# Kernel tuning notes

Hardware: AMD Instinct MI355X
Metric: run time of the kernel (lower is better)

## Reference

```python
import jax, jax.numpy as jnp
import numpy as np

B, S, D, H, F = 8, 1024, 1024, 16, 4096
DH = D // H  # 64
EPS = 1e-5


def layer_norm(x, g, b):
    mu = jnp.mean(x, axis=-1, keepdims=True)
    var = jnp.mean(jnp.square(x - mu), axis=-1, keepdims=True)
    return (x - mu) * jax.lax.rsqrt(var + EPS) * g + b


def mha(q_in, k_in, v_in, wq, wk, wv, wo, causal):
    # wq/wk/wv: [H, D, DH] (stacked per-head nn.Linear weights, pre-transposed)
    Q = jnp.einsum('bsd,hdk->bhsk', q_in, wq)
    K = jnp.einsum('bsd,hdk->bhsk', k_in, wk)
    V = jnp.einsum('bsd,hdk->bhsk', v_in, wv)
    scores = jnp.einsum('bhsk,bhtk->bhst', Q, K) / jnp.sqrt(jnp.asarray(DH, Q.dtype))
    if causal:
        mask = jnp.triu(jnp.ones((S, S), dtype=bool), k=1)  # True = inaccessible
        scores = jnp.where(mask, -jnp.inf, scores)
    A = jax.nn.softmax(scores, axis=-1)
    heads = jnp.einsum('bhst,bhtk->bhsk', A, V)
    heads = heads.transpose(0, 2, 1, 3).reshape(q_in.shape[0], q_in.shape[1], D)
    return heads @ wo.T  # nn.Linear convention


def setup_inputs() -> dict:
    key = jax.random.key(0)
    ks = jax.random.split(key, 16)
    sc = 1.0 / np.sqrt(D)
    scf = 1.0 / np.sqrt(F)
    return {
        'embeds': jax.random.normal(ks[0], (B, S, D), jnp.float32),
        'encoder_output': jax.random.normal(ks[1], (B, S, D), jnp.float32),
        'wq1': jax.random.normal(ks[2], (H, D, DH), jnp.float32) * sc,
        'wk1': jax.random.normal(ks[3], (H, D, DH), jnp.float32) * sc,
        'wv1': jax.random.normal(ks[4], (H, D, DH), jnp.float32) * sc,
        'wo1': jax.random.normal(ks[5], (D, D), jnp.float32) * sc,
        'wq2': jax.random.normal(ks[6], (H, D, DH), jnp.float32) * sc,
        'wk2': jax.random.normal(ks[7], (H, D, DH), jnp.float32) * sc,
        'wv2': jax.random.normal(ks[8], (H, D, DH), jnp.float32) * sc,
        'wo2': jax.random.normal(ks[9], (D, D), jnp.float32) * sc,
        'ln1_g': jnp.ones((D,), jnp.float32), 'ln1_b': jnp.zeros((D,), jnp.float32),
        'ln2_g': jnp.ones((D,), jnp.float32), 'ln2_b': jnp.zeros((D,), jnp.float32),
        'ln3_g': jnp.ones((D,), jnp.float32), 'ln3_b': jnp.zeros((D,), jnp.float32),
        'w1': jax.random.normal(ks[10], (F, D), jnp.float32) * sc,
        'b1': jnp.zeros((F,), jnp.float32),
        'w2': jax.random.normal(ks[11], (D, F), jnp.float32) * scf,
        'b2': jnp.zeros((D,), jnp.float32),
    }


def reference(embeds, encoder_output, wq1, wk1, wv1, wo1, wq2, wk2, wv2, wo2,
              ln1_g, ln1_b, ln2_g, ln2_b, ln3_g, ln3_b, w1, b1, w2, b2):
    # masked (causal) self-attention + residual + LN
    sa = mha(embeds, embeds, embeds, wq1, wk1, wv1, wo1, causal=True)
    x1 = layer_norm(sa + embeds, ln1_g, ln1_b)
    # cross-attention (no mask) + residual + LN
    ca = mha(x1, encoder_output, encoder_output, wq2, wk2, wv2, wo2, causal=False)
    x2 = layer_norm(ca + x1, ln2_g, ln2_b)
    # feedforward (Linear -> GELU(exact) -> Linear) + residual + LN
    ff = jax.nn.gelu(x2 @ w1.T + b1, approximate=False) @ w2.T + b2
    return layer_norm(ff + x2, ln3_g, ln3_b)
```

## Files before the change

kernel.cpp:

```cpp
#include <hip/hip_runtime.h>
#include <cstdint>
#include <cstddef>

typedef unsigned short u16;
typedef __attribute__((ext_vector_type(4))) float f32x4;
typedef __attribute__((ext_vector_type(4))) float f4;
typedef __attribute__((ext_vector_type(8))) short short8x;
typedef __attribute__((ext_vector_type(4))) u16 u16x4;
typedef __attribute__((ext_vector_type(8))) u16 u16x8;

#define DEV static __device__ __forceinline__

DEV void gl_lds16(const void* g, void* l) {
  __builtin_amdgcn_global_load_lds(
      (const __attribute__((address_space(1))) unsigned int*)g,
      (__attribute__((address_space(3))) unsigned int*)l, 16, 0, 0);
}

DEV u16 f2bf(float f) {
  unsigned u = __float_as_uint(f);
  u += 0x7fffu + ((u >> 16) & 1u);
  return (u16)(u >> 16);
}


__global__ __launch_bounds__(256) void cast_bf16(const float* __restrict__ X, u16* __restrict__ Y) {
  size_t i = ((size_t)blockIdx.x * 256 + threadIdx.x) * 4;
  f4 v = *(const f4*)(X + i);
  u16x4 y;
#pragma unroll
  for (int j = 0; j < 4; ++j) y[j] = f2bf(v[j]);
  *(u16x4*)(Y + i) = y;
}

__global__ __launch_bounds__(256) void cast_wqkv(const float* __restrict__ W, u16* __restrict__ Wt) {
  __shared__ float tile[64][65];
  const int t = threadIdx.x;
  const int h = blockIdx.y;
  const int d0 = blockIdx.x * 64;
  const float* Wb = W + (size_t)h * (1024 * 64);
  const int di = t >> 2;
  const int j0 = (t & 3) * 16;
#pragma unroll
  for (int c = 0; c < 4; ++c) {
    f4 v = *(const f4*)(Wb + (size_t)(d0 + di) * 64 + j0 + c * 4);
#pragma unroll
    for (int j = 0; j < 4; ++j) tile[di][j0 + c * 4 + j] = v[j];
  }
  __syncthreads();
  const int k = t >> 2;
  const int dd0 = (t & 3) * 16;
  u16x8 o0, o1;
#pragma unroll
  for (int u = 0; u < 8; ++u) o0[u] = f2bf(tile[dd0 + u][k]);
#pragma unroll
  for (int u = 0; u < 8; ++u) o1[u] = f2bf(tile[dd0 + 8 + u][k]);
  u16* dst = Wt + (size_t)(h * 64 + k) * 1024 + d0 + dd0;
  *(u16x8*)(dst) = o0;
  *(u16x8*)(dst + 8) = o1;
}

__global__ __launch_bounds__(256) void transpose_v(const u16* __restrict__ V, u16* __restrict__ Vt) {
  __shared__ u16 tile[32][72];
  const int t = threadIdx.x;
  const int bh = blockIdx.y;
  const int s0 = blockIdx.x * 32;
  const u16* Vb = V + (size_t)(bh >> 4) * (1024 * 1024) + (size_t)(bh & 15) * 64;
  const int si = t >> 3, d0 = (t & 7) * 8;
  u16x8 val = *(const u16x8*)(Vb + (size_t)(s0 + si) * 1024 + d0);
#pragma unroll
  for (int u = 0; u < 8; ++u) tile[si][d0 + u] = val[u];
  __syncthreads();
  const int d = t >> 2, sj0 = (t & 3) * 8;
  u16x8 o;
#pragma unroll
  for (int u = 0; u < 8; ++u) o[u] = tile[sj0 + u][d];
  *(u16x8*)(Vt + (size_t)bh * (64 * 1024) + (size_t)d * 1024 + s0 + sj0) = o;
}

template <int EPI>
__global__ __launch_bounds__(256, 2) void gemm_bt(const u16* __restrict__ A, const u16* __restrict__ Bt,
                                                  void* __restrict__ C, const float* __restrict__ bias,
                                                  int M, int N, int K) {
  __shared__ u16 As[2][128 * 32];
  __shared__ u16 Bs[2][128 * 32];
  const int t = threadIdx.x;
  const int wave = t >> 6, lane = t & 63;
  const int lr = lane & 15, lkg = lane >> 4, lk = lkg * 8;
  const int wr = (wave >> 1) * 64, wc = (wave & 1) * 64;
  const int m0 = blockIdx.y * 128, n0 = blockIdx.x * 128;

  const char* gA = (const char*)(A + (size_t)(m0 + (t >> 2)) * K) + ((t & 3) << 4);
  const char* gB = (const char*)(Bt + (size_t)(n0 + (t >> 2)) * K) + ((t & 3) << 4);
  const size_t rowskip = (size_t)64 * K * 2;

  const f32x4 fzero = {0.f, 0.f, 0.f, 0.f};
  f32x4 acc[4][4];
#pragma unroll
  for (int m = 0; m < 4; ++m)
#pragma unroll
    for (int n = 0; n < 4; ++n) acc[m][n] = fzero;

  const int nk = K >> 5;

  auto stage = [&](int buf, int kt) {
    const size_t kb = (size_t)kt * 64;
    char* la = ((char*)&As[buf][0]) + wave * 1024;
    char* lb = ((char*)&Bs[buf][0]) + wave * 1024;
    gl_lds16(gA + kb, la);
    gl_lds16(gA + kb + rowskip, la + 4096);
    gl_lds16(gB + kb, lb);
    gl_lds16(gB + kb + rowskip, lb + 4096);
  };

  auto compute = [&](int buf) {
    const u16* as = &As[buf][0];
    const u16* bs = &Bs[buf][0];
    short8x aF[4], bF[4];
#pragma unroll
    for (int m = 0; m < 4; ++m) aF[m] = *(const short8x*)(as + (wr + m * 16 + lr) * 32 + lk);
#pragma unroll
    for (int n = 0; n < 4; ++n) bF[n] = *(const short8x*)(bs + (wc + n * 16 + lr) * 32 + lk);
#pragma unroll
    for (int m = 0; m < 4; ++m)
#pragma unroll
      for (int n = 0; n < 4; ++n)
        acc[m][n] = __builtin_amdgcn_mfma_f32_16x16x32_bf16(aF[m], bF[n], acc[m][n], 0, 0, 0);
  };

  stage(0, 0);
  __syncthreads();
  int cur = 0;
  for (int kt = 0; kt < nk; ++kt) {
    if (kt + 1 < nk) stage(cur ^ 1, kt + 1);
    compute(cur);
    __syncthreads();
    cur ^= 1;
  }

#pragma unroll
  for (int m = 0; m < 4; ++m) {
#pragma unroll
    for (int rr = 0; rr < 4; ++rr) {
      const int gm = m0 + wr + m * 16 + lkg * 4 + rr;
#pragma unroll
      for (int n = 0; n < 4; ++n) {
        const int gn = n0 + wc + n * 16 + lr;
        float v = acc[m][n][rr];
        if (EPI == 2 || EPI == 3) v += bias[gn];
        if (EPI == 2) v = 0.5f * v * (1.0f + erff(v * 0.70710678118654752f));
        if (EPI == 4) v *= 0.125f;
        if (EPI == 0 || EPI == 2 || EPI == 4)
          ((u16*)C)[(size_t)gm * N + gn] = f2bf(v);
        else
          ((float*)C)[(size_t)gm * N + gn] = v;
      }
    }
  }
}

template <int CAUSAL>
__global__ __launch_bounds__(256, 2) void flash_attn(const u16* __restrict__ Q, const u16* __restrict__ Kk,
                                                     const u16* __restrict__ Vt, u16* __restrict__ O) {
  __shared__ u16 Ks[2][64 * 64];
  __shared__ u16 Vs[2][64 * 64];
  __shared__ u16 Ps[4][32 * 72];
  const int t = threadIdx.x;
  const int wave = t >> 6, lane = t & 63;
  const int lr = lane & 15, lkg = lane >> 4, lk = lkg * 8;
  const int sw = lr & 7;
  const int bh = blockIdx.y;
  const size_t base = (size_t)(bh >> 4) * (1024 * 1024) + (size_t)(bh & 15) * 64;
  const u16* Qb = Q + base;
  const u16* Kb = Kk + base;
  const u16* Vtb = Vt + (size_t)bh * (64 * 1024);
  u16* Ob = O + base;
  const int qt = blockIdx.x * 128;
  const int qw = qt + wave * 32;

  const f32x4 fzero = {0.f, 0.f, 0.f, 0.f};
  short8x qf[2][2];
#pragma unroll
  for (int rb = 0; rb < 2; ++rb)
#pragma unroll
    for (int kk = 0; kk < 2; ++kk)
      qf[rb][kk] = *(const short8x*)(Qb + (size_t)(qw + rb * 16 + lr) * 1024 + kk * 32 + lk);

  float m_[2][4], l_[2][4];
  f32x4 o_[2][4];
#pragma unroll
  for (int rb = 0; rb < 2; ++rb) {
#pragma unroll
    for (int rr = 0; rr < 4; ++rr) { m_[rb][rr] = -1e30f; l_[rb][rr] = 0.f; }
#pragma unroll
    for (int db = 0; db < 4; ++db) o_[rb][db] = fzero;
  }

  const int rsel = lane >> 3;
  const int csw = ((lane & 7) ^ rsel) << 4;

  auto stage = [&](int buf, int kv0) {
#pragma unroll
    for (int s = 0; s < 2; ++s) {
      const int row = s * 32 + wave * 8 + rsel;
      gl_lds16((const char*)Kb + (size_t)(kv0 + row) * 2048 + csw,
               (char*)&Ks[buf][0] + s * 4096 + wave * 1024);
      gl_lds16((const char*)Vtb + (size_t)row * 2048 + (size_t)kv0 * 2 + csw,
               (char*)&Vs[buf][0] + s * 4096 + wave * 1024);
    }
  };

  const int kv_end = CAUSAL ? (qt + 128) : 1024;
  const int nt = kv_end >> 6;

  stage(0, 0);
  __syncthreads();
  int cur = 0;
  for (int tt = 0; tt < nt; ++tt) {
    const int kv0 = tt * 64;
    if (tt + 1 < nt) stage(cur ^ 1, kv0 + 64);

    const char* ksb = (const char*)&Ks[cur][0];
    const char* vsb = (const char*)&Vs[cur][0];

    short8x kf[4][2];
#pragma unroll
    for (int nb = 0; nb < 4; ++nb) {
      const int row = nb * 16 + lr;
#pragma unroll
      for (int kk = 0; kk < 2; ++kk)
        kf[nb][kk] = *(const short8x*)(ksb + row * 128 + (((kk * 4 + lkg) ^ sw) << 4));
    }

#pragma unroll
    for (int rb = 0; rb < 2; ++rb) {
      f32x4 s[4];
#pragma unroll
      for (int nb = 0; nb < 4; ++nb) {
        s[nb] = __builtin_amdgcn_mfma_f32_16x16x32_bf16(qf[rb][0], kf[nb][0], fzero, 0, 0, 0);
        s[nb] = __builtin_amdgcn_mfma_f32_16x16x32_bf16(qf[rb][1], kf[nb][1], s[nb], 0, 0, 0);
      }
      if (CAUSAL && (kv0 + 63 > qw + rb * 16)) {
#pragma unroll
        for (int rr = 0; rr < 4; ++rr) {
          const int qg = qw + rb * 16 + lkg * 4 + rr;
#pragma unroll
          for (int nb = 0; nb < 4; ++nb)
            if (kv0 + nb * 16 + lr > qg) s[nb][rr] = -1e30f;
        }
      }
#pragma unroll
      for (int rr = 0; rr < 4; ++rr) {
        float mx = fmaxf(fmaxf(s[0][rr], s[1][rr]), fmaxf(s[2][rr], s[3][rr]));
#pragma unroll
        for (int d = 1; d < 16; d <<= 1) mx = fmaxf(mx, __shfl_xor(mx, d, 16));
        const float mold = m_[rb][rr];
        const float mnew = fmaxf(mold, mx);
        float p[4];
#pragma unroll
        for (int nb = 0; nb < 4; ++nb) p[nb] = __expf(s[nb][rr] - mnew);
        float rsum = (p[0] + p[1]) + (p[2] + p[3]);
#pragma unroll
        for (int d = 1; d < 16; d <<= 1) rsum += __shfl_xor(rsum, d, 16);
        const float alpha = __expf(mold - mnew);
        m_[rb][rr] = mnew;
        l_[rb][rr] = l_[rb][rr] * alpha + rsum;
#pragma unroll
        for (int db = 0; db < 4; ++db) o_[rb][db][rr] *= alpha;
        const int prow = rb * 16 + lkg * 4 + rr;
#pragma unroll
        for (int nb = 0; nb < 4; ++nb)
          Ps[wave][prow * 72 + nb * 16 + lr] = f2bf(p[nb]);
      }
    }
    asm volatile("s_waitcnt lgkmcnt(0)" ::: "memory");

    short8x vF[4][2];
#pragma unroll
    for (int db = 0; db < 4; ++db) {
      const int row = db * 16 + lr;
#pragma unroll
      for (int kk = 0; kk < 2; ++kk)
        vF[db][kk] = *(const short8x*)(vsb + row * 128 + (((kk * 4 + lkg) ^ sw) << 4));
    }
#pragma unroll
    for (int rb = 0; rb < 2; ++rb) {
#pragma unroll
      for (int kk = 0; kk < 2; ++kk) {
        const short8x aP = *(const short8x*)((const char*)&Ps[wave][0] + (rb * 16 + lr) * 144 + kk * 64 + lkg * 16);
#pragma unroll
        for (int db = 0; db < 4; ++db)
          o_[rb][db] = __builtin_amdgcn_mfma_f32_16x16x32_bf16(aP, vF[db][kk], o_[rb][db], 0, 0, 0);
      }
    }
    __syncthreads();
    cur ^= 1;
  }

#pragma unroll
  for (int rb = 0; rb < 2; ++rb)
#pragma unroll
    for (int rr = 0; rr < 4; ++rr) {
      const float inv = 1.0f / l_[rb][rr];
      const int qg = qw + rb * 16 + lkg * 4 + rr;
#pragma unroll
      for (int db = 0; db < 4; ++db)
        Ob[(size_t)qg * 1024 + db * 16 + lr] = f2bf(o_[rb][db][rr] * inv);
    }
}

__global__ __launch_bounds__(256) void ln_res(const float* __restrict__ X, const float* __restrict__ R,
                                              const float* __restrict__ gam, const float* __restrict__ bet,
                                              float* __restrict__ oF, u16* __restrict__ oB) {
  __shared__ float red[8];
  const int row = blockIdx.x, t = threadIdx.x;
  const int wave = t >> 6, lane = t & 63;
  const size_t off = (size_t)row * 1024 + t * 4;
  f4 x = *(const f4*)(X + off);
  f4 r = *(const f4*)(R + off);
  float v[4];
  float s = 0.f, sq = 0.f;
#pragma unroll
  for (int j = 0; j < 4; ++j) {
    v[j] = x[j] + r[j];
    s += v[j];
    sq += v[j] * v[j];
  }
#pragma unroll
  for (int d = 1; d < 64; d <<= 1) {
    s += __shfl_xor(s, d, 64);
    sq += __shfl_xor(sq, d, 64);
  }
  if (lane == 0) { red[wave * 2] = s; red[wave * 2 + 1] = sq; }
  __syncthreads();
  s = red[0] + red[2] + red[4] + red[6];
  sq = red[1] + red[3] + red[5] + red[7];
  const float mu = s * (1.0f / 1024.0f);
  const float var = sq * (1.0f / 1024.0f) - mu * mu;
  const float rs = rsqrtf(var + 1e-5f);
  f4 g4 = *(const f4*)(gam + t * 4);
  f4 b4 = *(const f4*)(bet + t * 4);
  f4 y;
#pragma unroll
  for (int j = 0; j < 4; ++j) y[j] = (v[j] - mu) * rs * g4[j] + b4[j];
  *(f4*)(oF + off) = y;
  if (oB) {
    u16x4 yb;
#pragma unroll
    for (int j = 0; j < 4; ++j) yb[j] = f2bf(y[j]);
    *(u16x4*)(oB + off) = yb;
  }
}

extern "C" void kernel_launch(void* const* d_in, const int* in_sizes, int n_in,
                              void* d_out, int out_size, void* d_ws, size_t ws_size,
                              hipStream_t stream) {
  const float* embeds = (const float*)d_in[0];
  const float* enc = (const float*)d_in[1];
  const float* wq1 = (const float*)d_in[2];
  const float* wk1 = (const float*)d_in[3];
  const float* wv1 = (const float*)d_in[4];
  const float* wo1 = (const float*)d_in[5];
  const float* wq2 = (const float*)d_in[6];
  const float* wk2 = (const float*)d_in[7];
  const float* wv2 = (const float*)d_in[8];
  const float* wo2 = (const float*)d_in[9];
  const float* ln1g = (const float*)d_in[10];
  const float* ln1b = (const float*)d_in[11];
  const float* ln2g = (const float*)d_in[12];
  const float* ln2b = (const float*)d_in[13];
  const float* ln3g = (const float*)d_in[14];
  const float* ln3b = (const float*)d_in[15];
  const float* w1 = (const float*)d_in[16];
  const float* b1 = (const float*)d_in[17];
  const float* w2 = (const float*)d_in[18];
  const float* b2 = (const float*)d_in[19];
  float* out = (float*)d_out;
  char* ws = (char*)d_ws;
  const size_t MB = (size_t)1 << 20;

  u16* Qb = (u16*)(ws + 0 * MB);
  u16* Kb = (u16*)(ws + 16 * MB);
  u16* Vb = (u16*)(ws + 32 * MB);
  u16* Vtb = (u16*)(ws + 48 * MB);
  u16* Hd = (u16*)(ws + 64 * MB);
  float* Of = (float*)(ws + 80 * MB);
  u16* ebf = (u16*)(ws + 112 * MB);
  u16* encb = (u16*)(ws + 128 * MB);
  float* x1f = (float*)(ws + 144 * MB);
  float* x2f = (float*)(ws + 176 * MB);
  u16* Wq1t = (u16*)(ws + 208 * MB);
  u16* Wk1t = (u16*)(ws + 210 * MB);
  u16* Wv1t = (u16*)(ws + 212 * MB);
  u16* Wo1b = (u16*)(ws + 214 * MB);
  u16* Wq2t = (u16*)(ws + 216 * MB);
  u16* Wk2t = (u16*)(ws + 218 * MB);
  u16* Wv2t = (u16*)(ws + 220 * MB);
  u16* Wo2b = (u16*)(ws + 222 * MB);
  u16* W1b = (u16*)(ws + 224 * MB);
  u16* W2b = (u16*)(ws + 232 * MB);
  u16* x1b = ebf;
  u16* x2b = encb;
  u16* Hff = (u16*)(ws + 0 * MB);

  dim3 blk(256);

  cast_bf16<<<8192, blk, 0, stream>>>(embeds, ebf);
  cast_bf16<<<8192, blk, 0, stream>>>(enc, encb);
  cast_wqkv<<<dim3(16, 16), blk, 0, stream>>>(wq1, Wq1t);
  cast_wqkv<<<dim3(16, 16), blk, 0, stream>>>(wk1, Wk1t);
  cast_wqkv<<<dim3(16, 16), blk, 0, stream>>>(wv1, Wv1t);
  cast_wqkv<<<dim3(16, 16), blk, 0, stream>>>(wq2, Wq2t);
  cast_wqkv<<<dim3(16, 16), blk, 0, stream>>>(wk2, Wk2t);
  cast_wqkv<<<dim3(16, 16), blk, 0, stream>>>(wv2, Wv2t);
  cast_bf16<<<1024, blk, 0, stream>>>(wo1, Wo1b);
  cast_bf16<<<1024, blk, 0, stream>>>(wo2, Wo2b);
  cast_bf16<<<4096, blk, 0, stream>>>(w1, W1b);
  cast_bf16<<<4096, blk, 0, stream>>>(w2, W2b);

  gemm_bt<4><<<dim3(8, 64), blk, 0, stream>>>(ebf, Wq1t, Qb, nullptr, 8192, 1024, 1024);
  gemm_bt<0><<<dim3(8, 64), blk, 0, stream>>>(ebf, Wk1t, Kb, nullptr, 8192, 1024, 1024);
  gemm_bt<0><<<dim3(8, 64), blk, 0, stream>>>(ebf, Wv1t, Vb, nullptr, 8192, 1024, 1024);
  transpose_v<<<dim3(32, 128), blk, 0, stream>>>(Vb, Vtb);
  flash_attn<1><<<dim3(8, 128), blk, 0, stream>>>(Qb, Kb, Vtb, Hd);
  gemm_bt<1><<<dim3(8, 64), blk, 0, stream>>>(Hd, Wo1b, Of, nullptr, 8192, 1024, 1024);
  ln_res<<<8192, blk, 0, stream>>>(Of, embeds, ln1g, ln1b, x1f, x1b);

  gemm_bt<4><<<dim3(8, 64), blk, 0, stream>>>(x1b, Wq2t, Qb, nullptr, 8192, 1024, 1024);
  gemm_bt<0><<<dim3(8, 64), blk, 0, stream>>>(encb, Wk2t, Kb, nullptr, 8192, 1024, 1024);
  gemm_bt<0><<<dim3(8, 64), blk, 0, stream>>>(encb, Wv2t, Vb, nullptr, 8192, 1024, 1024);
  transpose_v<<<dim3(32, 128), blk, 0, stream>>>(Vb, Vtb);
  flash_attn<0><<<dim3(8, 128), blk, 0, stream>>>(Qb, Kb, Vtb, Hd);
  gemm_bt<1><<<dim3(8, 64), blk, 0, stream>>>(Hd, Wo2b, Of, nullptr, 8192, 1024, 1024);
  ln_res<<<8192, blk, 0, stream>>>(Of, x1f, ln2g, ln2b, x2f, x2b);

  gemm_bt<2><<<dim3(32, 64), blk, 0, stream>>>(x2b, W1b, Hff, b1, 8192, 4096, 1024);
  gemm_bt<3><<<dim3(8, 64), blk, 0, stream>>>(Hff, W2b, Of, b2, 8192, 1024, 4096);
  ln_res<<<8192, blk, 0, stream>>>(Of, x2f, ln3g, ln3b, out, nullptr);
}
```

Measured before the change: 796.5 us.

## Fuse QKV projections into one GEMM, swizzle GEMM LDS, raise occupancy

Self-attention Q/K/V projections now run as a single GEMM with N=3072 writing into an interleaved QKV buffer, and cross-attention K/V become one N=2048 GEMM. The attention and transpose kernels take row strides so they can read directly from that buffer. The GEMM LDS layout gets an XOR swizzle on 16-byte chunks to cut bank conflicts, and launch bounds rise from 2 to 3 blocks per SM. The fused GEMM relies on the Wq/Wk/Wv transposed weights sitting contiguously in the workspace, 2 MB apart. The higher occupancy target may force register spills in the 4x4 accumulator tile.

```diff
diff --git a/kernel.cpp b/kernel.cpp
--- a/kernel.cpp
+++ b/kernel.cpp
@@ -60,14 +60,15 @@
   *(u16x8*)(dst + 8) = o1;
 }
 
-__global__ __launch_bounds__(256) void transpose_v(const u16* __restrict__ V, u16* __restrict__ Vt) {
+__global__ __launch_bounds__(256) void transpose_v(const u16* __restrict__ V, u16* __restrict__ Vt,
+                                                   int vstride, int voff) {
   __shared__ u16 tile[32][72];
   const int t = threadIdx.x;
   const int bh = blockIdx.y;
   const int s0 = blockIdx.x * 32;
-  const u16* Vb = V + (size_t)(bh >> 4) * (1024 * 1024) + (size_t)(bh & 15) * 64;
+  const u16* Vb = V + (size_t)(bh >> 4) * (1024 * (size_t)vstride) + voff + (bh & 15) * 64;
   const int si = t >> 3, d0 = (t & 7) * 8;
-  u16x8 val = *(const u16x8*)(Vb + (size_t)(s0 + si) * 1024 + d0);
+  u16x8 val = *(const u16x8*)(Vb + (size_t)(s0 + si) * vstride + d0);
 #pragma unroll
   for (int u = 0; u < 8; ++u) tile[si][d0 + u] = val[u];
   __syncthreads();
@@ -79,19 +80,21 @@
 }
 
 template <int EPI>
-__global__ __launch_bounds__(256, 2) void gemm_bt(const u16* __restrict__ A, const u16* __restrict__ Bt,
+__global__ __launch_bounds__(256, 3) void gemm_bt(const u16* __restrict__ A, const u16* __restrict__ Bt,
                                                   void* __restrict__ C, const float* __restrict__ bias,
-                                                  int M, int N, int K) {
+                                                  int M, int N, int K, int ldc) {
   __shared__ u16 As[2][128 * 32];
   __shared__ u16 Bs[2][128 * 32];
   const int t = threadIdx.x;
   const int wave = t >> 6, lane = t & 63;
-  const int lr = lane & 15, lkg = lane >> 4, lk = lkg * 8;
+  const int lr = lane & 15, lkg = lane >> 4;
+  const int swz = (lr >> 1) & 3;
   const int wr = (wave >> 1) * 64, wc = (wave & 1) * 64;
   const int m0 = blockIdx.y * 128, n0 = blockIdx.x * 128;
 
-  const char* gA = (const char*)(A + (size_t)(m0 + (t >> 2)) * K) + ((t & 3) << 4);
-  const char* gB = (const char*)(Bt + (size_t)(n0 + (t >> 2)) * K) + ((t & 3) << 4);
+  const int schunk = ((t & 3) ^ ((t >> 3) & 3)) << 4;
+  const char* gA = (const char*)(A + (size_t)(m0 + (t >> 2)) * K) + schunk;
+  const char* gB = (const char*)(Bt + (size_t)(n0 + (t >> 2)) * K) + schunk;
   const size_t rowskip = (size_t)64 * K * 2;
 
   const f32x4 fzero = {0.f, 0.f, 0.f, 0.f};
@@ -114,13 +117,15 @@
   };
 
   auto compute = [&](int buf) {
-    const u16* as = &As[buf][0];
-    const u16* bs = &Bs[buf][0];
+    const char* as = (const char*)&As[buf][0];
+    const char* bs = (const char*)&Bs[buf][0];
     short8x aF[4], bF[4];
 #pragma unroll
-    for (int m = 0; m < 4; ++m) aF[m] = *(const short8x*)(as + (wr + m * 16 + lr) * 32 + lk);
-#pragma unroll
-    for (int n = 0; n < 4; ++n) bF[n] = *(const short8x*)(bs + (wc + n * 16 + lr) * 32 + lk);
+    for (int m = 0; m < 4; ++m)
+      aF[m] = *(const short8x*)(as + (size_t)(wr + m * 16 + lr) * 64 + ((lkg ^ swz) << 4));
+#pragma unroll
+    for (int n = 0; n < 4; ++n)
+      bF[n] = *(const short8x*)(bs + (size_t)(wc + n * 16 + lr) * 64 + ((lkg ^ swz) << 4));
 #pragma unroll
     for (int m = 0; m < 4; ++m)
 #pragma unroll
@@ -150,10 +155,11 @@
         if (EPI == 2 || EPI == 3) v += bias[gn];
         if (EPI == 2) v = 0.5f * v * (1.0f + erff(v * 0.70710678118654752f));
         if (EPI == 4) v *= 0.125f;
-        if (EPI == 0 || EPI == 2 || EPI == 4)
-          ((u16*)C)[(size_t)gm * N + gn] = f2bf(v);
+        if (EPI == 5 && gn < 1024) v *= 0.125f;
+        if (EPI == 1 || EPI == 3)
+          ((float*)C)[(size_t)gm * ldc + gn] = v;
         else
-          ((float*)C)[(size_t)gm * N + gn] = v;
+          ((u16*)C)[(size_t)gm * ldc + gn] = f2bf(v);
       }
     }
   }
@@ -161,7 +167,8 @@
 
 template <int CAUSAL>
 __global__ __launch_bounds__(256, 2) void flash_attn(const u16* __restrict__ Q, const u16* __restrict__ Kk,
-                                                     const u16* __restrict__ Vt, u16* __restrict__ O) {
+                                                     const u16* __restrict__ Vt, u16* __restrict__ O,
+                                                     int qst) {
   __shared__ u16 Ks[2][64 * 64];
   __shared__ u16 Vs[2][64 * 64];
   __shared__ u16 Ps[4][32 * 72];
@@ -170,11 +177,11 @@
   const int lr = lane & 15, lkg = lane >> 4, lk = lkg * 8;
   const int sw = lr & 7;
   const int bh = blockIdx.y;
-  const size_t base = (size_t)(bh >> 4) * (1024 * 1024) + (size_t)(bh & 15) * 64;
+  const size_t base = (size_t)(bh >> 4) * (1024 * (size_t)qst) + (bh & 15) * 64;
   const u16* Qb = Q + base;
   const u16* Kb = Kk + base;
   const u16* Vtb = Vt + (size_t)bh * (64 * 1024);
-  u16* Ob = O + base;
+  u16* Ob = O + (size_t)(bh >> 4) * (1024 * 1024) + (bh & 15) * 64;
   const int qt = blockIdx.x * 128;
   const int qw = qt + wave * 32;
 
@@ -184,7 +191,7 @@
   for (int rb = 0; rb < 2; ++rb)
 #pragma unroll
     for (int kk = 0; kk < 2; ++kk)
-      qf[rb][kk] = *(const short8x*)(Qb + (size_t)(qw + rb * 16 + lr) * 1024 + kk * 32 + lk);
+      qf[rb][kk] = *(const short8x*)(Qb + (size_t)(qw + rb * 16 + lr) * qst + kk * 32 + lk);
 
   float m_[2][4], l_[2][4];
   f32x4 o_[2][4];
@@ -203,7 +210,7 @@
 #pragma unroll
     for (int s = 0; s < 2; ++s) {
       const int row = s * 32 + wave * 8 + rsel;
-      gl_lds16((const char*)Kb + (size_t)(kv0 + row) * 2048 + csw,
+      gl_lds16((const char*)Kb + (size_t)(kv0 + row) * (size_t)(qst * 2) + csw,
                (char*)&Ks[buf][0] + s * 4096 + wave * 1024);
       gl_lds16((const char*)Vtb + (size_t)row * 2048 + (size_t)kv0 * 2 + csw,
                (char*)&Vs[buf][0] + s * 4096 + wave * 1024);
@@ -379,9 +386,7 @@
   char* ws = (char*)d_ws;
   const size_t MB = (size_t)1 << 20;
 
-  u16* Qb = (u16*)(ws + 0 * MB);
-  u16* Kb = (u16*)(ws + 16 * MB);
-  u16* Vb = (u16*)(ws + 32 * MB);
+  u16* QKV = (u16*)(ws + 0 * MB);
   u16* Vtb = (u16*)(ws + 48 * MB);
   u16* Hd = (u16*)(ws + 64 * MB);
   float* Of = (float*)(ws + 80 * MB);
@@ -418,23 +423,20 @@
   cast_bf16<<<4096, blk, 0, stream>>>(w1, W1b);
   cast_bf16<<<4096, blk, 0, stream>>>(w2, W2b);
 
-  gemm_bt<4><<<dim3(8, 64), blk, 0, stream>>>(ebf, Wq1t, Qb, nullptr, 8192, 1024, 1024);
-  gemm_bt<0><<<dim3(8, 64), blk, 0, stream>>>(ebf, Wk1t, Kb, nullptr, 8192, 1024, 1024);
-  gemm_bt<0><<<dim3(8, 64), blk, 0, stream>>>(ebf, Wv1t, Vb, nullptr, 8192, 1024, 1024);
-  transpose_v<<<dim3(32, 128), blk, 0, stream>>>(Vb, Vtb);
-  flash_attn<1><<<dim3(8, 128), blk, 0, stream>>>(Qb, Kb, Vtb, Hd);
-  gemm_bt<1><<<dim3(8, 64), blk, 0, stream>>>(Hd, Wo1b, Of, nullptr, 8192, 1024, 1024);
+  gemm_bt<5><<<dim3(24, 64), blk, 0, stream>>>(ebf, Wq1t, QKV, nullptr, 8192, 3072, 1024, 3072);
+  transpose_v<<<dim3(32, 128), blk, 0, stream>>>(QKV, Vtb, 3072, 2048);
+  flash_attn<1><<<dim3(8, 128), blk, 0, stream>>>(QKV, QKV + 1024, Vtb, Hd, 3072);
+  gemm_bt<1><<<dim3(8, 64), blk, 0, stream>>>(Hd, Wo1b, Of, nullptr, 8192, 1024, 1024, 1024);
   ln_res<<<8192, blk, 0, stream>>>(Of, embeds, ln1g, ln1b, x1f, x1b);
 
-  gemm_bt<4><<<dim3(8, 64), blk, 0, stream>>>(x1b, Wq2t, Qb, nullptr, 8192, 1024, 1024);
-  gemm_bt<0><<<dim3(8, 64), blk, 0, stream>>>(encb, Wk2t, Kb, nullptr, 8192, 1024, 1024);
-  gemm_bt<0><<<dim3(8, 64), blk, 0, stream>>>(encb, Wv2t, Vb, nullptr, 8192, 1024, 1024);
-  transpose_v<<<dim3(32, 128), blk, 0, stream>>>(Vb, Vtb);
-  flash_attn<0><<<dim3(8, 128), blk, 0, stream>>>(Qb, Kb, Vtb, Hd);
-  gemm_bt<1><<<dim3(8, 64), blk, 0, stream>>>(Hd, Wo2b, Of, nullptr, 8192, 1024, 1024);
+  gemm_bt<4><<<dim3(8, 64), blk, 0, stream>>>(x1b, Wq2t, QKV, nullptr, 8192, 1024, 1024, 3072);
+  gemm_bt<0><<<dim3(16, 64), blk, 0, stream>>>(encb, Wk2t, QKV + 1024, nullptr, 8192, 2048, 1024, 3072);
+  transpose_v<<<dim3(32, 128), blk, 0, stream>>>(QKV, Vtb, 3072, 2048);
+  flash_attn<0><<<dim3(8, 128), blk, 0, stream>>>(QKV, QKV + 1024, Vtb, Hd, 3072);
+  gemm_bt<1><<<dim3(8, 64), blk, 0, stream>>>(Hd, Wo2b, Of, nullptr, 8192, 1024, 1024, 1024);
   ln_res<<<8192, blk, 0, stream>>>(Of, x1f, ln2g, ln2b, x2f, x2b);
 
-  gemm_bt<2><<<dim3(32, 64), blk, 0, stream>>>(x2b, W1b, Hff, b1, 8192, 4096, 1024);
-  gemm_bt<3><<<dim3(8, 64), blk, 0, stream>>>(Hff, W2b, Of, b2, 8192, 1024, 4096);
+  gemm_bt<2><<<dim3(32, 64), blk, 0, stream>>>(x2b, W1b, Hff, b1, 8192, 4096, 1024, 4096);
+  gemm_bt<3><<<dim3(8, 64), blk, 0, stream>>>(Hff, W2b, Of, b2, 8192, 1024, 4096, 1024);
   ln_res<<<8192, blk, 0, stream>>>(Of, x2f, ln3g, ln3b, out, nullptr);
 }
```

New measurement: 762.8 us. -4.2%, faster.
